# Kernel tuning notes

Measured on AMD Instinct MI355X. Metric: run time of the kernel, lower is better.

Reference implementation:

```python
import jax, jax.numpy as jnp
import numpy as np

B, N, W = 4, 4096, 1024
H, A, P = 16, 64, 64


def setup_inputs() -> dict:
    key = jax.random.key(0)
    ks = jax.random.split(key, 11)
    u = lambda k, shape: jax.random.uniform(k, shape, jnp.float32, -0.05, 0.05)  # keras 'random_uniform'
    glorot_v = (2.0 / (W + A)) ** 0.5
    return {
        'x': jax.random.normal(ks[0], (B, N, W), jnp.float32),
        'k1': u(ks[1], (H, W)),
        'k2': u(ks[2], (H, W)),
        'k3': u(ks[3], (H, W)),
        'a1': u(ks[4], (H, P, 1)),
        'a2': u(ks[5], (H, P, 1)),
        'b1': u(ks[6], (H, P, 1)),
        'b2': u(ks[7], (H, P, 1)),
        'c': u(ks[8], (H, P, 1)),
        'value_weight': jax.random.normal(ks[9], (H, W, A), jnp.float32) * glorot_v,
        'output_weight': jax.random.normal(ks[10], (H, W, A), jnp.float32) * glorot_v,
    }


def reference(x, k1, k2, k3, a1, a2, b1, b2, c, value_weight, output_weight):
    n = jnp.linspace(0.0, 1.0, x.shape[-2])                      # [N]
    p1 = jnp.sum(jnp.sin(a1 * n + b1) * c, axis=-2)              # [H,N]
    p2 = jnp.sum(jnp.sin(a2 * n + b2) * c, axis=-2)              # [H,N]
    cross = jnp.einsum('bnw,hw->bhn', x, k1) + p1                # [B,H,N]
    diag = jnp.einsum('bnw,hw->bhn', x, k2)
    extra = jnp.einsum('bnw,hw->bhn', x, k3)
    values = jnp.einsum('bnw,hwa->bhna', x, value_weight)        # [B,H,N,A]
    cexp = lambda z: jnp.exp(jnp.clip(z, -20.0, 20.0))[..., None]
    cross, diag, extra = cexp(cross), cexp(diag), cexp(extra)    # [B,H,N,1]
    p2e = cexp(p2)                                               # [H,N,1]
    num = jnp.cumsum(cross * values, axis=2) * p2e * extra + values * diag
    den = jnp.cumsum(cross, axis=2) * p2e * extra + diag
    out = num / den                                              # [B,H,N,A]
    return jnp.einsum('bhna,hwa->bnw', out, output_weight)       # [B,N,W]
```

## Files before the change

### kernel.cpp

```cpp
#include <hip/hip_runtime.h>
#include <hip/hip_bf16.h>
#include <stdint.h>

typedef __hip_bfloat16 bf16;
typedef __attribute__((ext_vector_type(8))) short short8;
typedef __attribute__((ext_vector_type(4))) float floatx4;

#define Bb 4
#define Nn 4096
#define Ww 1024
#define Hh 16
#define Aa 64
#define Pp 64
#define Jj 64
#define Ll 64

__device__ __forceinline__ float clamp20(float z){ return fminf(fmaxf(z, -20.0f), 20.0f); }
__device__ __forceinline__ float b2f(unsigned short u){ return __uint_as_float((unsigned)u << 16); }
__device__ __forceinline__ unsigned short f2b(float f){
    bf16 t = __float2bfloat16(f);
    return *reinterpret_cast<unsigned short*>(&t);
}

__device__ __forceinline__ void gl_lds16(const bf16* g, bf16* l){
    __builtin_amdgcn_global_load_lds((const __attribute__((address_space(1))) void*)g,
                                     (__attribute__((address_space(3))) void*)l, 16, 0, 0);
}


__global__ __launch_bounds__(256) void prep_w(
    const float* __restrict__ k1, const float* __restrict__ k2, const float* __restrict__ k3,
    const float* __restrict__ vw, const float* __restrict__ ow,
    bf16* __restrict__ Ktp, bf16* __restrict__ VWt, bf16* __restrict__ OWt){
    const int blk = blockIdx.x, tid = threadIdx.x;
    if (blk < 256){
        __shared__ float tile[64][65];
        const int h = blk >> 4, w0 = (blk & 15) * 64;
#pragma unroll
        for (int p = 0; p < 4; ++p){
            int wr = p * 16 + (tid >> 4);
            int a4 = (tid & 15) * 4;
            float4 v = *(const float4*)(vw + (h << 16) + ((w0 + wr) << 6) + a4);
            tile[wr][a4 + 0] = v.x; tile[wr][a4 + 1] = v.y;
            tile[wr][a4 + 2] = v.z; tile[wr][a4 + 3] = v.w;
        }
        __syncthreads();
#pragma unroll
        for (int p = 0; p < 4; ++p){
            int ar = p * 16 + (tid >> 4);
            int w4 = (tid & 15) * 4;
            ushort4 o = make_ushort4(f2b(tile[w4 + 0][ar]), f2b(tile[w4 + 1][ar]),
                                     f2b(tile[w4 + 2][ar]), f2b(tile[w4 + 3][ar]));
            *(ushort4*)(VWt + (size_t)(h * 64 + ar) * 1024 + w0 + w4) = o;
        }
    } else if (blk < 1280){
        int idx = (blk - 256) * 256 + tid;
        int base = idx * 4;
        int w = base >> 10, r0 = base & 1023;
        int h = r0 >> 6, a0 = r0 & 63;
        float4 v = *(const float4*)(ow + (h << 16) + (w << 6) + a0);
        *(ushort4*)(OWt + base) = make_ushort4(f2b(v.x), f2b(v.y), f2b(v.z), f2b(v.w));
    } else {
        int idx = (blk - 1280) * 256 + tid;
        int base = idx * 4;
        int r = base >> 10, k = base & 1023;
        float4 v = make_float4(0.f, 0.f, 0.f, 0.f);
        if (r < 16)      v = *(const float4*)(k1 + r * 1024 + k);
        else if (r < 32) v = *(const float4*)(k2 + (r - 16) * 1024 + k);
        else if (r < 48) v = *(const float4*)(k3 + (r - 32) * 1024 + k);
        *(ushort4*)(Ktp + base) = make_ushort4(f2b(v.x), f2b(v.y), f2b(v.z), f2b(v.w));
    }
}

__global__ __launch_bounds__(256) void prep_sin(
    const float* __restrict__ a1, const float* __restrict__ a2,
    const float* __restrict__ b1, const float* __restrict__ b2,
    const float* __restrict__ c,
    float* __restrict__ p1, float* __restrict__ p2e){
    __shared__ float sa1[64], sa2[64], sb1[64], sb2[64], scf[64];
    const int blk = blockIdx.x, tid = threadIdx.x;
    const int h = blk >> 4;
    if (tid < 64){
        sa1[tid] = a1[h * 64 + tid];
        sa2[tid] = a2[h * 64 + tid];
        sb1[tid] = b1[h * 64 + tid];
        sb2[tid] = b2[h * 64 + tid];
        scf[tid] = c [h * 64 + tid];
    }
    __syncthreads();
    const int idx = blk * 256 + tid;
    const int i = idx & (Nn - 1);
    float t = (float)i * (1.0f / (float)(Nn - 1));
    float s1 = 0.f, s2 = 0.f;
#pragma unroll 8
    for (int p = 0; p < Pp; ++p){
        float cv = scf[p];
        s1 += __sinf(sa1[p] * t + sb1[p]) * cv;
        s2 += __sinf(sa2[p] * t + sb2[p]) * cv;
    }
    p1[idx]  = s1;
    p2e[idx] = expf(clamp20(s2));
}

__global__ __launch_bounds__(256) void proj_gemm(const float* __restrict__ X,
                                                 const bf16* __restrict__ Ktp,
                                                 const float* __restrict__ p1,
                                                 bf16* __restrict__ xb,
                                                 float* __restrict__ cross_e,
                                                 float* __restrict__ diag_e,
                                                 float* __restrict__ extra_e){
    __shared__ bf16 As[64 * 32];
    __shared__ bf16 Bs[64 * 32];
    const int tid  = threadIdx.x;
    const int wave = tid >> 6, lane = tid & 63;
    const int m0 = blockIdx.x * 64;

    const int lrow = lane >> 2;
    const int scol = (lane & 3) * 8;
    const int srow = wave * 16 + lrow;
    const float* Xg = X + (size_t)(m0 + srow) * 1024 + scol;
    const bf16*  Bg = Ktp + (size_t)srow * 1024 + scol;
    bf16* xbg = xb + (size_t)(m0 + srow) * 1024 + scol;
    bf16* Al = As + (size_t)(wave * 16 + lrow) * 32 + (lane & 3) * 8;
    bf16* Bl = Bs + (wave * 16) * 32;

    floatx4 acc[3] = {};
    const int fr = lane & 15;
    const int fk = (lane >> 4) * 8;

    for (int k0 = 0; k0 < 1024; k0 += 32){
        gl_lds16(Bg + k0, Bl);
        float4 v0 = *(const float4*)(Xg + k0);
        float4 v1 = *(const float4*)(Xg + k0 + 4);
        union { ushort4 u4[2]; short8 s8; } pk;
        pk.u4[0] = make_ushort4(f2b(v0.x), f2b(v0.y), f2b(v0.z), f2b(v0.w));
        pk.u4[1] = make_ushort4(f2b(v1.x), f2b(v1.y), f2b(v1.z), f2b(v1.w));
        *(short8*)Al = pk.s8;
        *(short8*)(xbg + k0) = pk.s8;
        __syncthreads();
        short8 af = *(const short8*)&As[(wave * 16 + fr) * 32 + fk];
        short8 bfr[3];
#pragma unroll
        for (int j = 0; j < 3; ++j)
            bfr[j] = *(const short8*)&Bs[(j * 16 + fr) * 32 + fk];
#pragma unroll
        for (int j = 0; j < 3; ++j)
            acc[j] = __builtin_amdgcn_mfma_f32_16x16x32_bf16(af, bfr[j], acc[j], 0, 0, 0);
        __syncthreads();
    }

    const int cr = (lane >> 4) * 4;
#pragma unroll
    for (int j = 0; j < 3; ++j){
        float* dst = (j == 0) ? cross_e : (j == 1) ? diag_e : extra_e;
#pragma unroll
        for (int r = 0; r < 4; ++r){
            int row = m0 + wave * 16 + cr + r;
            int n = row & (Nn - 1), b = row >> 12;
            float s = acc[j][r];
            if (j == 0) s += p1[fr * Nn + n];
            dst[(b * Hh + fr) * Nn + n] = expf(clamp20(s));
        }
    }
}

__device__ __forceinline__ void stage_q(const bf16* srcTileBase, int K, bf16* ldsQuarter, int tid){
    int r  = tid >> 3;
    int col = (((tid & 7) ^ (r & 7)) << 3);
    gl_lds16(srcTileBase + (size_t)r * K + col, ldsQuarter + (tid >> 6) * 512);
}

template<int WRITE_BF16>
__global__ __launch_bounds__(512) void gemm256(const bf16* __restrict__ A,
                                               const bf16* __restrict__ Bt,
                                               void* __restrict__ Cv,
                                               int M, int N, int K){
    __shared__ bf16 ldsA[2][256 * 64];
    __shared__ bf16 ldsB[2][256 * 64];
    const int tid  = threadIdx.x;
    const int wave = tid >> 6, lane = tid & 63;

    const int flat = blockIdx.y * gridDim.x + blockIdx.x;
    const int nwg  = gridDim.x * gridDim.y;
    const int cpx  = nwg >> 3;
    const int swz  = (flat & 7) * cpx + (flat >> 3);
    const int m0 = (swz / gridDim.x) * 256, n0 = (swz % gridDim.x) * 256;
    const int wm = (wave >> 2) * 128, wn = (wave & 3) * 64;
    const int fr = lane & 15, quad = lane >> 4;
    const int nt = K >> 6;

    floatx4 acc[8][4] = {};

#pragma unroll
    for (int q = 0; q < 4; ++q)
        stage_q(A  + (size_t)(m0 + q * 64) * K, K, &ldsA[0][q * 4096], tid);
#pragma unroll
    for (int q = 0; q < 4; ++q)
        stage_q(Bt + (size_t)(n0 + q * 64) * K, K, &ldsB[0][q * 4096], tid);
#pragma unroll
    for (int q = 0; q < 4; ++q)
        stage_q(Bt + (size_t)(n0 + q * 64) * K + 64, K, &ldsB[1][q * 4096], tid);
    stage_q(A + (size_t)(m0 +   0) * K + 64, K, &ldsA[1][0 * 4096], tid);
    stage_q(A + (size_t)(m0 + 128) * K + 64, K, &ldsA[1][2 * 4096], tid);

    for (int t = 0; t < nt; ++t){
        if (t == nt - 1) asm volatile("s_waitcnt vmcnt(0)" ::: "memory");
        else             asm volatile("s_waitcnt vmcnt(6)" ::: "memory");
        __builtin_amdgcn_sched_barrier(0);
        __builtin_amdgcn_s_barrier();
        __builtin_amdgcn_sched_barrier(0);

        const bf16* Abuf = ldsA[t & 1];
        const bf16* Bbuf = ldsB[t & 1];
        short8 bfr[4][2];

#pragma unroll
        for (int p = 0; p < 4; ++p){
            short8 af[2][2];
#pragma unroll
            for (int ii = 0; ii < 2; ++ii){
                int R = wm + (2 * p + ii) * 16 + fr;
#pragma unroll
                for (int kc = 0; kc < 2; ++kc){
                    int lb = kc * 4 + quad;
                    af[ii][kc] = *(const short8*)&Abuf[R * 64 + ((lb ^ (R & 7)) << 3)];
                }
            }
            if (p == 0){
#pragma unroll
                for (int j = 0; j < 4; ++j){
                    int R = wn + j * 16 + fr;
#pragma unroll
                    for (int kc = 0; kc < 2; ++kc){
                        int lb = kc * 4 + quad;
                        bfr[j][kc] = *(const short8*)&Bbuf[R * 64 + ((lb ^ (R & 7)) << 3)];
                    }
                }
            }
            if (p == 0 && t + 1 < nt){
                bf16* d = ldsA[(t + 1) & 1];
                stage_q(A + (size_t)(m0 +  64) * K + (size_t)(t + 1) * 64, K, d + 1 * 4096, tid);
                stage_q(A + (size_t)(m0 + 192) * K + (size_t)(t + 1) * 64, K, d + 3 * 4096, tid);
            }
            if (p == 1 && t + 2 < nt){
                bf16* d = ldsB[t & 1];
                stage_q(Bt + (size_t)(n0 +   0) * K + (size_t)(t + 2) * 64, K, d + 0 * 4096, tid);
                stage_q(Bt + (size_t)(n0 +  64) * K + (size_t)(t + 2) * 64, K, d + 1 * 4096, tid);
            }
            if (p == 2 && t + 2 < nt){
                bf16* d = ldsB[t & 1];
                stage_q(Bt + (size_t)(n0 + 128) * K + (size_t)(t + 2) * 64, K, d + 2 * 4096, tid);
                stage_q(Bt + (size_t)(n0 + 192) * K + (size_t)(t + 2) * 64, K, d + 3 * 4096, tid);
            }
            if (p == 3 && t + 2 < nt){
                bf16* d = ldsA[t & 1];
                stage_q(A + (size_t)(m0 +   0) * K + (size_t)(t + 2) * 64, K, d + 0 * 4096, tid);
                stage_q(A + (size_t)(m0 + 128) * K + (size_t)(t + 2) * 64, K, d + 2 * 4096, tid);
            }
            __builtin_amdgcn_s_setprio(1);
#pragma unroll
            for (int ii = 0; ii < 2; ++ii)
#pragma unroll
                for (int j = 0; j < 4; ++j)
#pragma unroll
                    for (int kc = 0; kc < 2; ++kc)
                        acc[2 * p + ii][j] = __builtin_amdgcn_mfma_f32_16x16x32_bf16(
                            af[ii][kc], bfr[j][kc], acc[2 * p + ii][j], 0, 0, 0);
            __builtin_amdgcn_s_setprio(0);
            if (p == 0 || p == 1){
                __builtin_amdgcn_s_barrier();
                __builtin_amdgcn_sched_barrier(0);
            }
        }
    }

    const int cr = quad * 4;
#pragma unroll
    for (int i = 0; i < 8; ++i)
#pragma unroll
        for (int j = 0; j < 4; ++j){
            int row = m0 + wm + i * 16 + cr;
            int col = n0 + wn + j * 16 + fr;
            if (WRITE_BF16){
                bf16* C = (bf16*)Cv;
#pragma unroll
                for (int r = 0; r < 4; ++r)
                    C[(size_t)(row + r) * N + col] = __float2bfloat16(acc[i][j][r]);
            } else {
                float* C = (float*)Cv;
#pragma unroll
                for (int r = 0; r < 4; ++r)
                    C[(size_t)(row + r) * N + col] = acc[i][j][r];
            }
        }
}

__global__ __launch_bounds__(64) void scan1(const bf16* __restrict__ values,
                                            const float* __restrict__ cross_e,
                                            float* __restrict__ csum_c, float* __restrict__ csum_cv){
    const int blk = blockIdx.x;
    const int j = blk & (Jj - 1);
    const int bh = blk >> 6;
    const int h = bh & (Hh - 1), b = bh >> 4;
    const int lane = threadIdx.x;
    const int tq = lane >> 4;
    const int a4 = (lane & 15) << 2;
    const float* cp = cross_e + bh * Nn + j * Ll;
    float sc = 0.f, s0 = 0.f, s1 = 0.f, s2 = 0.f, s3 = 0.f;
#pragma unroll
    for (int i = 0; i < 16; ++i){
        int t = tq * 16 + i;
        int n = j * Ll + t;
        float ce = cp[t];
        ushort4 pv = *(const ushort4*)(values + (((size_t)(b * Nn + n)) << 10) + (h << 6) + a4);
        sc += ce;
        s0 += ce * b2f(pv.x); s1 += ce * b2f(pv.y);
        s2 += ce * b2f(pv.z); s3 += ce * b2f(pv.w);
    }
    sc += __shfl_xor(sc, 16); sc += __shfl_xor(sc, 32);
    s0 += __shfl_xor(s0, 16); s0 += __shfl_xor(s0, 32);
    s1 += __shfl_xor(s1, 16); s1 += __shfl_xor(s1, 32);
    s2 += __shfl_xor(s2, 16); s2 += __shfl_xor(s2, 32);
    s3 += __shfl_xor(s3, 16); s3 += __shfl_xor(s3, 32);
    if (lane == 0) csum_c[blk] = sc;
    if (tq == 0){
        float4 o = make_float4(s0, s1, s2, s3);
        *(float4*)(csum_cv + (blk << 6) + a4) = o;
    }
}

__global__ __launch_bounds__(64) void scan2(const float* __restrict__ csum_c,
                                            const float* __restrict__ csum_cv,
                                            float* __restrict__ pref_c, float* __restrict__ pref_cv){
    const int bh = blockIdx.x;
    const int lane = threadIdx.x;
    float rc = 0.f, rcv = 0.f;
    for (int j = 0; j < Jj; ++j){
        int idx = bh * Jj + j;
        if (lane == 0) pref_c[idx] = rc;
        pref_cv[(idx << 6) + lane] = rcv;
        rc  += csum_c[idx];
        rcv += csum_cv[(idx << 6) + lane];
    }
}

__global__ __launch_bounds__(64) void scan3(const bf16* __restrict__ values,
                                            const float* __restrict__ cross_e,
                                            const float* __restrict__ diag_e,
                                            const float* __restrict__ extra_e,
                                            const float* __restrict__ p2e,
                                            const float* __restrict__ pref_c,
                                            const float* __restrict__ pref_cv,
                                            bf16* __restrict__ out2){
    const int blk = blockIdx.x;
    const int j = blk & (Jj - 1);
    const int bh = blk >> 6;
    const int h = bh & (Hh - 1), b = bh >> 4;
    const int lane = threadIdx.x;
    const int tq = lane >> 4;
    const int al = lane & 15;
    const int a4 = al << 2;
    const float* cp = cross_e + bh * Nn + j * Ll;
    const float* dp = diag_e  + bh * Nn + j * Ll;
    const float* ep = extra_e + bh * Nn + j * Ll;
    const float* pp = p2e + h * Nn + j * Ll;

    ushort4 pv[16];
    float cef[16];
    float lc = 0.f, l0 = 0.f, l1 = 0.f, l2 = 0.f, l3 = 0.f;
#pragma unroll
    for (int i = 0; i < 16; ++i){
        int t = tq * 16 + i;
        int n = j * Ll + t;
        cef[i] = cp[t];
        pv[i] = *(const ushort4*)(values + (((size_t)(b * Nn + n)) << 10) + (h << 6) + a4);
        float ce = cef[i];
        lc += ce;
        l0 += ce * b2f(pv[i].x); l1 += ce * b2f(pv[i].y);
        l2 += ce * b2f(pv[i].z); l3 += ce * b2f(pv[i].w);
    }

    float rc = pref_c[blk];
    float4 pcv = *(const float4*)(pref_cv + (blk << 6) + a4);
    float r0 = pcv.x, r1 = pcv.y, r2 = pcv.z, r3 = pcv.w;
#pragma unroll
    for (int g = 0; g < 3; ++g){
        int src = g * 16 + al;
        float oc = __shfl(lc, src);
        float o0 = __shfl(l0, src), o1 = __shfl(l1, src);
        float o2 = __shfl(l2, src), o3 = __shfl(l3, src);
        if (tq > g){ rc += oc; r0 += o0; r1 += o1; r2 += o2; r3 += o3; }
    }

#pragma unroll
    for (int i = 0; i < 16; ++i){
        int t = tq * 16 + i;
        int n = j * Ll + t;
        float ce = cef[i], de = dp[t], ee = ep[t], pe = pp[t];
        float v0 = b2f(pv[i].x), v1 = b2f(pv[i].y);
        float v2 = b2f(pv[i].z), v3 = b2f(pv[i].w);
        rc += ce;
        r0 += ce * v0; r1 += ce * v1; r2 += ce * v2; r3 += ce * v3;
        float pee = pe * ee;
        float invd = 1.0f / (rc * pee + de);
        ushort4 o;
        o.x = f2b((r0 * pee + v0 * de) * invd);
        o.y = f2b((r1 * pee + v1 * de) * invd);
        o.z = f2b((r2 * pee + v2 * de) * invd);
        o.w = f2b((r3 * pee + v3 * de) * invd);
        *(ushort4*)(out2 + (((size_t)(b * Nn + n)) << 10) + (h << 6) + a4) = o;
    }
}

extern "C" void kernel_launch(void* const* d_in, const int* in_sizes, int n_in,
                              void* d_out, int out_size, void* d_ws, size_t ws_size,
                              hipStream_t stream){
    const float* x  = (const float*)d_in[0];
    const float* k1 = (const float*)d_in[1];
    const float* k2 = (const float*)d_in[2];
    const float* k3 = (const float*)d_in[3];
    const float* a1 = (const float*)d_in[4];
    const float* a2 = (const float*)d_in[5];
    const float* b1 = (const float*)d_in[6];
    const float* b2 = (const float*)d_in[7];
    const float* c  = (const float*)d_in[8];
    const float* vw = (const float*)d_in[9];
    const float* ow = (const float*)d_in[10];
    float* out = (float*)d_out;

    char* p = (char*)d_ws;
    auto alloc = [&](size_t bytes) -> void* {
        void* r = (void*)p;
        p += (bytes + 255) & ~(size_t)255;
        return r;
    };
    bf16*  xb      = (bf16*) alloc((size_t)Bb * Nn * Ww * 2);
    bf16*  Ktp     = (bf16*) alloc((size_t)64 * Ww * 2);
    bf16*  VWt     = (bf16*) alloc((size_t)Hh * Aa * Ww * 2);
    bf16*  OWt     = (bf16*) alloc((size_t)Ww * Hh * Aa * 2);
    float* p1      = (float*)alloc((size_t)Hh * Nn * 4);
    float* p2e     = (float*)alloc((size_t)Hh * Nn * 4);
    float* cross_e = (float*)alloc((size_t)Bb * Hh * Nn * 4);
    float* diag_e  = (float*)alloc((size_t)Bb * Hh * Nn * 4);
    float* extra_e = (float*)alloc((size_t)Bb * Hh * Nn * 4);
    float* csum_c  = (float*)alloc((size_t)Bb * Hh * Jj * 4);
    float* pref_c  = (float*)alloc((size_t)Bb * Hh * Jj * 4);
    float* csum_cv = (float*)alloc((size_t)Bb * Hh * Jj * Aa * 4);
    float* pref_cv = (float*)alloc((size_t)Bb * Hh * Jj * Aa * 4);
    bf16*  values  = (bf16*) alloc((size_t)Bb * Nn * Hh * Aa * 2);
    bf16*  out2    = (bf16*) alloc((size_t)Bb * Nn * Hh * Aa * 2);

    prep_w  <<<1344, 256, 0, stream>>>(k1, k2, k3, vw, ow, Ktp, VWt, OWt);
    prep_sin<<<256, 256, 0, stream>>>(a1, a2, b1, b2, c, p1, p2e);
    proj_gemm<<<(Bb * Nn) / 64, 256, 0, stream>>>(x, Ktp, p1, xb, cross_e, diag_e, extra_e);
    gemm256<1><<<dim3((Hh * Aa) / 256, (Bb * Nn) / 256), 512, 0, stream>>>(xb, VWt, (void*)values, Bb * Nn, Hh * Aa, Ww);
    scan1<<<Bb * Hh * Jj, 64, 0, stream>>>(values, cross_e, csum_c, csum_cv);
    scan2<<<Bb * Hh, 64, 0, stream>>>(csum_c, csum_cv, pref_c, pref_cv);
    scan3<<<Bb * Hh * Jj, 64, 0, stream>>>(values, cross_e, diag_e, extra_e, p2e, pref_c, pref_cv, out2);
    gemm256<0><<<dim3(Ww / 256, (Bb * Nn) / 256), 512, 0, stream>>>(out2, OWt, (void*)out, Bb * Nn, Ww, Hh * Aa);
}
```

Baseline: 264.9 us.

## Double-buffer LDS and prefetch X two tiles ahead in projection GEMM

Rewrites the projection GEMM main loop to use double-buffered LDS tiles, with X loads issued two iterations ahead and the K-tile async copy issued one ahead. Manual vmcnt/lgkmcnt waits and a single barrier per iteration replace the two __syncthreads. The goal is to overlap global-memory latency with MFMA work. The hand-tuned waitcnt counts are fragile: the vmcnt(2) assumes a particular number of outstanding loads, including the bf16 xb stores, and a miscount could cause races or stalls.

```diff
diff --git a/kernel.cpp b/kernel.cpp
--- a/kernel.cpp
+++ b/kernel.cpp
@@ -109,8 +109,8 @@
                                                  float* __restrict__ cross_e,
                                                  float* __restrict__ diag_e,
                                                  float* __restrict__ extra_e){
-    __shared__ bf16 As[64 * 32];
-    __shared__ bf16 Bs[64 * 32];
+    __shared__ bf16 As[2][64 * 32];
+    __shared__ bf16 Bs[2][64 * 32];
     const int tid  = threadIdx.x;
     const int wave = tid >> 6, lane = tid & 63;
     const int m0 = blockIdx.x * 64;
@@ -121,32 +121,58 @@
     const float* Xg = X + (size_t)(m0 + srow) * 1024 + scol;
     const bf16*  Bg = Ktp + (size_t)srow * 1024 + scol;
     bf16* xbg = xb + (size_t)(m0 + srow) * 1024 + scol;
-    bf16* Al = As + (size_t)(wave * 16 + lrow) * 32 + (lane & 3) * 8;
-    bf16* Bl = Bs + (wave * 16) * 32;
+    const int aoff = (wave * 16 + lrow) * 32 + (lane & 3) * 8;
+    const int boff = (wave * 16) * 32;
 
     floatx4 acc[3] = {};
     const int fr = lane & 15;
     const int fk = (lane >> 4) * 8;
-
-    for (int k0 = 0; k0 < 1024; k0 += 32){
-        gl_lds16(Bg + k0, Bl);
-        float4 v0 = *(const float4*)(Xg + k0);
-        float4 v1 = *(const float4*)(Xg + k0 + 4);
+    const int nt = 32;
+
+    float4 va0 = *(const float4*)(Xg + 0);
+    float4 va1 = *(const float4*)(Xg + 4);
+    float4 vb0 = *(const float4*)(Xg + 32);
+    float4 vb1 = *(const float4*)(Xg + 36);
+    gl_lds16(Bg + 0, &Bs[0][boff]);
+
+    for (int t = 0; t < nt; ++t){
+        const int k0 = t * 32;
+        if (t == 0 || t == nt - 1) asm volatile("s_waitcnt vmcnt(0)" ::: "memory");
+        else                       asm volatile("s_waitcnt vmcnt(2)" ::: "memory");
+        __builtin_amdgcn_sched_barrier(0);
+
         union { ushort4 u4[2]; short8 s8; } pk;
-        pk.u4[0] = make_ushort4(f2b(v0.x), f2b(v0.y), f2b(v0.z), f2b(v0.w));
-        pk.u4[1] = make_ushort4(f2b(v1.x), f2b(v1.y), f2b(v1.z), f2b(v1.w));
-        *(short8*)Al = pk.s8;
+        pk.u4[0] = make_ushort4(f2b(va0.x), f2b(va0.y), f2b(va0.z), f2b(va0.w));
+        pk.u4[1] = make_ushort4(f2b(va1.x), f2b(va1.y), f2b(va1.z), f2b(va1.w));
+        *(short8*)&As[t & 1][aoff] = pk.s8;
         *(short8*)(xbg + k0) = pk.s8;
-        __syncthreads();
-        short8 af = *(const short8*)&As[(wave * 16 + fr) * 32 + fk];
+
+        asm volatile("s_waitcnt lgkmcnt(0)" ::: "memory");
+        __builtin_amdgcn_sched_barrier(0);
+        __builtin_amdgcn_s_barrier();
+        __builtin_amdgcn_sched_barrier(0);
+
+        if (t + 1 < nt)
+            gl_lds16(Bg + k0 + 32, &Bs[(t + 1) & 1][boff]);
+        float4 nv0, nv1;
+        const bool pf = (t + 2 < nt);
+        if (pf){
+            nv0 = *(const float4*)(Xg + k0 + 64);
+            nv1 = *(const float4*)(Xg + k0 + 68);
+        }
+        __builtin_amdgcn_sched_barrier(0);
+
+        short8 af = *(const short8*)&As[t & 1][(wave * 16 + fr) * 32 + fk];
         short8 bfr[3];
 #pragma unroll
         for (int j = 0; j < 3; ++j)
-            bfr[j] = *(const short8*)&Bs[(j * 16 + fr) * 32 + fk];
+            bfr[j] = *(const short8*)&Bs[t & 1][(j * 16 + fr) * 32 + fk];
 #pragma unroll
         for (int j = 0; j < 3; ++j)
             acc[j] = __builtin_amdgcn_mfma_f32_16x16x32_bf16(af, bfr[j], acc[j], 0, 0, 0);
-        __syncthreads();
+
+        va0 = vb0; va1 = vb1;
+        if (pf){ vb0 = nv0; vb1 = nv1; }
     }
 
     const int cr = (lane >> 4) * 4;
```

Result: no change. 267.5 us (+1.0%).

## Software-pipeline proj_gemm with double-buffered K tiles and register-prefetched X

Applied to the files above, without the earlier changes.

Rewrites the projection GEMM main loop to work on 128-wide K tiles with two in-flight stages. X is loaded straight into registers two tiles ahead, then converted to bf16 and fed directly as MFMA A fragments, so the A tile no longer goes through LDS. The B (Ktp) tile is double-buffered in LDS with an XOR swizzle, and the loop uses manual vmcnt/lgkmcnt waits and sched barriers. The goal is to hide global-load latency and cut the number of barriers. In exchange it uses more registers and relies on hand-tuned wait counts, which are fragile.

```diff
diff --git a/kernel.cpp b/kernel.cpp
--- a/kernel.cpp
+++ b/kernel.cpp
@@ -109,47 +109,88 @@
                                                  float* __restrict__ cross_e,
                                                  float* __restrict__ diag_e,
                                                  float* __restrict__ extra_e){
-    __shared__ bf16 As[64 * 32];
-    __shared__ bf16 Bs[64 * 32];
+    __shared__ bf16 Bs[2][48 * 128];
     const int tid  = threadIdx.x;
     const int wave = tid >> 6, lane = tid & 63;
     const int m0 = blockIdx.x * 64;
-
-    const int lrow = lane >> 2;
-    const int scol = (lane & 3) * 8;
-    const int srow = wave * 16 + lrow;
-    const float* Xg = X + (size_t)(m0 + srow) * 1024 + scol;
-    const bf16*  Bg = Ktp + (size_t)srow * 1024 + scol;
-    bf16* xbg = xb + (size_t)(m0 + srow) * 1024 + scol;
-    bf16* Al = As + (size_t)(wave * 16 + lrow) * 32 + (lane & 3) * 8;
-    bf16* Bl = Bs + (wave * 16) * 32;
+    const int fr = lane & 15, quad = lane >> 4;
+
+    const float* Xf = X  + (size_t)(m0 + wave * 16 + fr) * 1024 + quad * 8;
+    bf16*       xbf = xb + (size_t)(m0 + wave * 16 + fr) * 1024 + quad * 8;
 
     floatx4 acc[3] = {};
-    const int fr = lane & 15;
-    const int fk = (lane >> 4) * 8;
-
-    for (int k0 = 0; k0 < 1024; k0 += 32){
-        gl_lds16(Bg + k0, Bl);
-        float4 v0 = *(const float4*)(Xg + k0);
-        float4 v1 = *(const float4*)(Xg + k0 + 4);
-        union { ushort4 u4[2]; short8 s8; } pk;
-        pk.u4[0] = make_ushort4(f2b(v0.x), f2b(v0.y), f2b(v0.z), f2b(v0.w));
-        pk.u4[1] = make_ushort4(f2b(v1.x), f2b(v1.y), f2b(v1.z), f2b(v1.w));
-        *(short8*)Al = pk.s8;
-        *(short8*)(xbg + k0) = pk.s8;
-        __syncthreads();
-        short8 af = *(const short8*)&As[(wave * 16 + fr) * 32 + fk];
-        short8 bfr[3];
+    float4 xA[8], xB[8];
+
+    auto loadX = [&](float4 (&d)[8], int t){
+#pragma unroll
+        for (int i = 0; i < 4; ++i){
+            d[2 * i]     = *(const float4*)(Xf + t * 128 + 32 * i);
+            d[2 * i + 1] = *(const float4*)(Xf + t * 128 + 32 * i + 4);
+        }
+    };
+    auto stageB = [&](int t){
+        bf16* base = &Bs[t & 1][0];
+#pragma unroll
+        for (int s = 0; s < 3; ++s){
+            int c = tid + s * 256;
+            int row = c >> 4, pch = c & 15;
+            int gcol = (pch ^ (row & 7)) << 3;
+            gl_lds16(Ktp + (size_t)row * 1024 + t * 128 + gcol,
+                     base + (size_t)(wave * 64 + s * 256) * 8);
+        }
+    };
+    auto iter = [&](int t, float4 (&xc_)[8], int vmN){
+        if (vmN == 0)       asm volatile("s_waitcnt vmcnt(0)"  ::: "memory");
+        else if (vmN == 11) asm volatile("s_waitcnt vmcnt(11)" ::: "memory");
+        else                asm volatile("s_waitcnt vmcnt(15)" ::: "memory");
+        __builtin_amdgcn_sched_barrier(0);
+        short8 afr[4];
+#pragma unroll
+        for (int i = 0; i < 4; ++i){
+            union { ushort4 u4[2]; short8 s8; } pk;
+            pk.u4[0] = make_ushort4(f2b(xc_[2*i].x),   f2b(xc_[2*i].y),
+                                    f2b(xc_[2*i].z),   f2b(xc_[2*i].w));
+            pk.u4[1] = make_ushort4(f2b(xc_[2*i+1].x), f2b(xc_[2*i+1].y),
+                                    f2b(xc_[2*i+1].z), f2b(xc_[2*i+1].w));
+            afr[i] = pk.s8;
+            *(short8*)(xbf + t * 128 + i * 32) = pk.s8;
+        }
+        __builtin_amdgcn_sched_barrier(0);
+        __builtin_amdgcn_s_barrier();
+        __builtin_amdgcn_sched_barrier(0);
+        short8 bfr[3][4];
 #pragma unroll
         for (int j = 0; j < 3; ++j)
-            bfr[j] = *(const short8*)&Bs[(j * 16 + fr) * 32 + fk];
-#pragma unroll
-        for (int j = 0; j < 3; ++j)
-            acc[j] = __builtin_amdgcn_mfma_f32_16x16x32_bf16(af, bfr[j], acc[j], 0, 0, 0);
-        __syncthreads();
-    }
-
-    const int cr = (lane >> 4) * 4;
+#pragma unroll
+            for (int i = 0; i < 4; ++i){
+                int R = j * 16 + fr;
+                int pch = (4 * i + quad) ^ (R & 7);
+                bfr[j][i] = *(const short8*)&Bs[t & 1][R * 128 + pch * 8];
+            }
+        asm volatile("s_waitcnt lgkmcnt(0)" ::: "memory");
+        __builtin_amdgcn_sched_barrier(0);
+        __builtin_amdgcn_s_barrier();
+        __builtin_amdgcn_sched_barrier(0);
+        if (t + 2 < 8){ loadX(xc_, t + 2); stageB(t + 2); }
+        __builtin_amdgcn_sched_barrier(0);
+#pragma unroll
+        for (int i = 0; i < 4; ++i)
+#pragma unroll
+            for (int j = 0; j < 3; ++j)
+                acc[j] = __builtin_amdgcn_mfma_f32_16x16x32_bf16(afr[i], bfr[j][i], acc[j], 0, 0, 0);
+    };
+
+    loadX(xA, 0); stageB(0);
+    loadX(xB, 1); stageB(1);
+    __builtin_amdgcn_sched_barrier(0);
+
+#pragma unroll
+    for (int tt = 0; tt < 4; ++tt){
+        iter(2 * tt,     xA, (tt == 0) ? 11 : 15);
+        iter(2 * tt + 1, xB, (tt == 3) ? 0  : 15);
+    }
+
+    const int cr = quad * 4;
 #pragma unroll
     for (int j = 0; j < 3; ++j){
         float* dst = (j == 0) ? cross_e : (j == 1) ? diag_e : extra_e;
```

New measurement: 257.7 us. 2.7% less time.
